# Optimization experiments

Hardware: AMD Instinct MI355X
Metric: run time of the kernel (lower is better)

Reference implementation:

```python
import jax, jax.numpy as jnp
import numpy as np

DIM = 1024
HEADS = 16
DIM_HEAD = 64
CHUNK = 64
INNER = HEADS * DIM_HEAD  # 1024


def setup_inputs() -> dict:
    key = jax.random.key(0)
    k1, k2, k3 = jax.random.split(key, 3)
    x = jax.random.normal(k1, (4, 4096, DIM), dtype=jnp.float32)
    # nn.Linear weights stored as (out, in); apply as x @ W.T
    w_qkv = jax.random.normal(k2, (INNER * 3, DIM), dtype=jnp.float32) * (DIM ** -0.5)
    w_out = jax.random.normal(k3, (DIM, INNER), dtype=jnp.float32) * (INNER ** -0.5)
    b_out = jnp.zeros((DIM,), dtype=jnp.float32)
    return {"x": x, "w_qkv": w_qkv, "w_out": w_out, "b_out": b_out}


def reference(x, w_qkv, w_out, b_out):
    b, n, _ = x.shape
    scale = DIM_HEAD ** -0.5
    qkv = jnp.einsum('bnd,ed->bne', x, w_qkv)  # (b, n, 3*inner)
    q, k, v = jnp.split(qkv, 3, axis=-1)
    nblk = n // CHUNK

    def to_blocks(t):
        # (b, n, h*d) -> (b, h, nblk, c, d)
        t = t.reshape(b, n, HEADS, DIM_HEAD).transpose(0, 2, 1, 3)
        return t.reshape(b, HEADS, nblk, CHUNK, DIM_HEAD)

    qb, kb, vb = to_blocks(q), to_blocks(k), to_blocks(v)
    scores = jnp.einsum('bhgqd,bhgkd->bhgqk', qb, kb) * scale  # block-local
    attn = jax.nn.softmax(scores, axis=-1)
    ob = jnp.einsum('bhgqk,bhgkd->bhgqd', attn, vb)
    out = ob.reshape(b, HEADS, n, DIM_HEAD).transpose(0, 2, 1, 3).reshape(b, n, INNER)
    return jnp.einsum('bne,de->bnd', out, w_out) + b_out
```

## Files before the change

kernel.cpp:

```cpp
#include <hip/hip_runtime.h>
#include <stdint.h>

typedef __attribute__((ext_vector_type(8))) short bf16x8;
typedef __attribute__((ext_vector_type(4))) float f32x4;

__device__ __forceinline__ unsigned short bf16_of(float f) {
  union { float f; uint32_t u; } x; x.f = f;
  uint32_t r = x.u + 0x7fffu + ((x.u >> 16) & 1u);
  return (unsigned short)(r >> 16);
}

#define GLD16(gp, lp) __builtin_amdgcn_global_load_lds( \
    (const __attribute__((address_space(1))) uint32_t*)(gp), \
    (__attribute__((address_space(3))) uint32_t*)(lp), 16, 0, 0)

#define BAR() do { asm volatile("" ::: "memory"); __builtin_amdgcn_s_barrier(); asm volatile("" ::: "memory"); } while (0)

__global__ void cvt_f32_bf16(const float* __restrict__ src,
                             unsigned short* __restrict__ dst, int n4) {
  int i = blockIdx.x * blockDim.x + threadIdx.x;
  int stride = gridDim.x * blockDim.x;
  for (int j = i; j < n4; j += stride) {
    float4 f = ((const float4*)src)[j];
    union { unsigned short s[4]; uint2 v; } u;
    u.s[0] = bf16_of(f.x); u.s[1] = bf16_of(f.y);
    u.s[2] = bf16_of(f.z); u.s[3] = bf16_of(f.w);
    ((uint2*)dst)[j] = u.v;
  }
}

template<int BIAS, int OUTF32, int GW, int NSEG>
__global__ __launch_bounds__(512, 2)
void gemm256f(const unsigned short* __restrict__ A,
              const unsigned short* __restrict__ B,
              void* __restrict__ C, const float* __restrict__ bias,
              int N, int K)
{
  __shared__ __align__(1024) unsigned short sm[65536];
  char* const smb = (char*)sm;
  const int tid = threadIdx.x, w = tid >> 6, lane = tid & 63;
  const int wm = w >> 2, wn = w & 3;
  const int fr = lane & 15, kg = lane >> 4;
  const int swz = (fr & 7) << 4;
  const int srow = lane >> 3, sslot = lane & 7;
  const int cXcd = blockIdx.x & 7, iIdx = blockIdx.x >> 3;
  const int NT_tot = NSEG * 16;

  auto tileMN = [&](int s, int& mt, int& nt) {
    const int T = cXcd * (32 * NSEG) + s * 32 + iIdx;
    const int g = T / (64 * GW), rr = T % (64 * GW);
    mt = rr / GW; nt = g * GW + rr % GW;
  };

  auto STAGE = [&](int u, int opnd, int half) {
    int mt, nt; tileMN(u >> 4, mt, nt);
    const unsigned short* G_ = opnd ? B : A;
    const int grow0 = (opnd ? nt : mt) << 8;
    char* region = smb + opnd * 65536 + (u & 1) * 32768 + half * 16384;
    const int k0 = (u & 15) << 6;
    #pragma unroll
    for (int i2 = 0; i2 < 2; ++i2) {
      const int c = i2 * 8 + w;
      const int row = half * 128 + c * 8 + srow;
      const int slot = sslot ^ srow;
      GLD16(G_ + (size_t)(grow0 + row) * K + k0 + slot * 8, region + c * 1024);
    }
  };
  auto LDA = [&](char* Ab, int j, int ks) -> bf16x8 {
    const int r = 32 * j + 16 * wm + fr;
    return *(const bf16x8*)(Ab + r * 128 + ((ks * 64 + kg * 16) ^ swz));
  };
  auto LDB = [&](char* Bb, int l, int ks) -> bf16x8 {
    const int r = 64 * l + 16 * wn + fr;
    return *(const bf16x8*)(Bb + r * 128 + ((ks * 64 + kg * 16) ^ swz));
  };

  f32x4 acc[8][4] = {};

  STAGE(0, 1, 0); STAGE(0, 0, 0); STAGE(0, 1, 1); STAGE(0, 0, 1);

  for (int s = 0; s < NSEG; ++s) {
    for (int tt = 0; tt < 16; ++tt) {
      const int T = s * 16 + tt;
      char* Ab = smb + (T & 1) * 32768;
      char* Bb = smb + 65536 + (T & 1) * 32768;
      bf16x8 a[4][2], b0[2][2], b1[2][2];

      asm volatile("s_waitcnt vmcnt(2)" ::: "memory");
      BAR();

      if (T + 1 < NT_tot) {
        STAGE(T + 1, 1, 0);
        STAGE(T + 1, 0, 0);
        STAGE(T + 1, 1, 1);
        STAGE(T + 1, 0, 1);
      }

      #pragma unroll
      for (int l = 0; l < 2; ++l) { b0[l][0] = LDB(Bb, l, 0); b0[l][1] = LDB(Bb, l, 1); }
      #pragma unroll
      for (int j = 0; j < 4; ++j) { a[j][0] = LDA(Ab, j, 0); a[j][1] = LDA(Ab, j, 1); }
      #pragma unroll
      for (int l = 0; l < 2; ++l) { b1[l][0] = LDB(Bb, l + 2, 0); b1[l][1] = LDB(Bb, l + 2, 1); }
      __builtin_amdgcn_s_setprio(1);
      #pragma unroll
      for (int j = 0; j < 4; ++j)
        #pragma unroll
        for (int l = 0; l < 2; ++l) {
          acc[j][l] = __builtin_amdgcn_mfma_f32_16x16x32_bf16(a[j][0], b0[l][0], acc[j][l], 0, 0, 0);
          acc[j][l] = __builtin_amdgcn_mfma_f32_16x16x32_bf16(a[j][1], b0[l][1], acc[j][l], 0, 0, 0);
        }
      #pragma unroll
      for (int j = 0; j < 4; ++j)
        #pragma unroll
        for (int l = 0; l < 2; ++l) {
          acc[j][l + 2] = __builtin_amdgcn_mfma_f32_16x16x32_bf16(a[j][0], b1[l][0], acc[j][l + 2], 0, 0, 0);
          acc[j][l + 2] = __builtin_amdgcn_mfma_f32_16x16x32_bf16(a[j][1], b1[l][1], acc[j][l + 2], 0, 0, 0);
        }
      __builtin_amdgcn_s_setprio(0);

      asm volatile("s_waitcnt vmcnt(8)" ::: "memory");
      BAR();

      #pragma unroll
      for (int j = 0; j < 4; ++j) { a[j][0] = LDA(Ab, j + 4, 0); a[j][1] = LDA(Ab, j + 4, 1); }
      __builtin_amdgcn_s_setprio(1);
      #pragma unroll
      for (int j = 0; j < 4; ++j)
        #pragma unroll
        for (int l = 0; l < 2; ++l) {
          acc[j + 4][l + 2] = __builtin_amdgcn_mfma_f32_16x16x32_bf16(a[j][0], b1[l][0], acc[j + 4][l + 2], 0, 0, 0);
          acc[j + 4][l + 2] = __builtin_amdgcn_mfma_f32_16x16x32_bf16(a[j][1], b1[l][1], acc[j + 4][l + 2], 0, 0, 0);
        }
      #pragma unroll
      for (int j = 0; j < 4; ++j)
        #pragma unroll
        for (int l = 0; l < 2; ++l) {
          acc[j + 4][l] = __builtin_amdgcn_mfma_f32_16x16x32_bf16(a[j][0], b0[l][0], acc[j + 4][l], 0, 0, 0);
          acc[j + 4][l] = __builtin_amdgcn_mfma_f32_16x16x32_bf16(a[j][1], b0[l][1], acc[j + 4][l], 0, 0, 0);
        }
      __builtin_amdgcn_s_setprio(0);
    }

    int mt, nt; tileMN(s, mt, nt);
    const int bm0 = mt << 8, bn0 = nt << 8;
    #pragma unroll
    for (int l = 0; l < 4; ++l) {
      const int col = bn0 + 64 * l + 16 * wn + fr;
      float bb = 0.0f;
      if (BIAS && OUTF32) bb = bias[col];
      #pragma unroll
      for (int j = 0; j < 8; ++j) {
        const int row0 = bm0 + 32 * j + 16 * wm + kg * 4;
        #pragma unroll
        for (int rr = 0; rr < 4; ++rr) {
          if (OUTF32)
            ((float*)C)[(size_t)(row0 + rr) * N + col] = acc[j][l][rr] + bb;
          else
            ((unsigned short*)C)[(size_t)(row0 + rr) * N + col] = bf16_of(acc[j][l][rr]);
        }
      }
    }
    #pragma unroll
    for (int j = 0; j < 8; ++j)
      #pragma unroll
      for (int l = 0; l < 4; ++l)
        acc[j][l] = f32x4{0.f, 0.f, 0.f, 0.f};
  }
}

__global__ __launch_bounds__(256, 2)
void attn_block(const unsigned short* __restrict__ qkv,
                unsigned short* __restrict__ o)
{
  __shared__ __align__(1024) unsigned short Qs[64 * 64];
  __shared__ __align__(1024) unsigned short Ks[64 * 64];
  __shared__ __align__(1024) unsigned short Vt[64 * 64];
  __shared__ __align__(1024) unsigned short Ps[64 * 64];
  const int tid = threadIdx.x, w = tid >> 6, lane = tid & 63;
  const int g = blockIdx.x, h = blockIdx.y, b = blockIdx.z;
  const size_t mbase = (size_t)b * 4096 + (size_t)g * 64;
  const unsigned short* qg = qkv + mbase * 3072 + h * 64;
  const unsigned short* kgl = qkv + mbase * 3072 + 1024 + h * 64;
  const unsigned short* vg = qkv + mbase * 3072 + 2048 + h * 64;

  #pragma unroll
  for (int i = 0; i < 2; ++i) {
    const int chunk = i * 4 + w;
    const int row = chunk * 8 + (lane >> 3);
    const int c8 = (lane & 7) ^ (row & 7);
    GLD16(qg + (size_t)row * 3072 + c8 * 8, (char*)Qs + chunk * 1024);
    GLD16(kgl + (size_t)row * 3072 + c8 * 8, (char*)Ks + chunk * 1024);
  }
  #pragma unroll
  for (int i = 0; i < 2; ++i) {
    const int c = i * 256 + tid;
    const int n = c >> 3, d0 = (c & 7) * 8;
    bf16x8 v = *(const bf16x8*)(vg + (size_t)n * 3072 + d0);
    #pragma unroll
    for (int j = 0; j < 8; ++j) {
      const int d = d0 + j;
      const int bo = d * 128 + n * 2;
      *(unsigned short*)((char*)Vt + (bo ^ ((d & 7) << 4))) = (unsigned short)v[j];
    }
  }
  __syncthreads();

  const int fr = lane & 15, kg = lane >> 4;
  f32x4 s[4] = {};
  #pragma unroll
  for (int kt = 0; kt < 2; ++kt) {
    const int kb = kt * 64 + kg * 16;
    const int rq = w * 16 + fr;
    bf16x8 aq = *(const bf16x8*)((const char*)Qs + rq * 128 + (kb ^ ((rq & 7) << 4)));
    #pragma unroll
    for (int nf = 0; nf < 4; ++nf) {
      const int rk = nf * 16 + fr;
      bf16x8 bk = *(const bf16x8*)((const char*)Ks + rk * 128 + (kb ^ ((rk & 7) << 4)));
      s[nf] = __builtin_amdgcn_mfma_f32_16x16x32_bf16(aq, bk, s[nf], 0, 0, 0);
    }
  }

  const float scale = 0.125f;
  float inv[4];
  #pragma unroll
  for (int r = 0; r < 4; ++r) {
    float m0 = fmaxf(fmaxf(s[0][r], s[1][r]), fmaxf(s[2][r], s[3][r]));
    #pragma unroll
    for (int d = 1; d < 16; d <<= 1) m0 = fmaxf(m0, __shfl_xor(m0, d));
    float sum = 0.0f;
    #pragma unroll
    for (int nf = 0; nf < 4; ++nf) {
      float p = __expf((s[nf][r] - m0) * scale);
      s[nf][r] = p;
      sum += p;
    }
    #pragma unroll
    for (int d = 1; d < 16; d <<= 1) sum += __shfl_xor(sum, d);
    inv[r] = 1.0f / sum;
  }

  #pragma unroll
  for (int r = 0; r < 4; ++r) {
    const int m = w * 16 + kg * 4 + r;
    #pragma unroll
    for (int nf = 0; nf < 4; ++nf) {
      const int bo = m * 128 + (nf * 16 + fr) * 2;
      *(unsigned short*)((char*)Ps + (bo ^ ((m & 7) << 4))) = bf16_of(s[nf][r] * inv[r]);
    }
  }
  __syncthreads();

  f32x4 oa[4] = {};
  #pragma unroll
  for (int kt = 0; kt < 2; ++kt) {
    const int kb = kt * 64 + kg * 16;
    const int rp = w * 16 + fr;
    bf16x8 ap = *(const bf16x8*)((const char*)Ps + rp * 128 + (kb ^ ((rp & 7) << 4)));
    #pragma unroll
    for (int df = 0; df < 4; ++df) {
      const int rv = df * 16 + fr;
      bf16x8 bv = *(const bf16x8*)((const char*)Vt + rv * 128 + (kb ^ ((rv & 7) << 4)));
      oa[df] = __builtin_amdgcn_mfma_f32_16x16x32_bf16(ap, bv, oa[df], 0, 0, 0);
    }
  }
  #pragma unroll
  for (int df = 0; df < 4; ++df) {
    #pragma unroll
    for (int r = 0; r < 4; ++r) {
      const size_t row = mbase + w * 16 + kg * 4 + r;
      const int col = h * 64 + df * 16 + fr;
      o[row * 1024 + col] = bf16_of(oa[df][r]);
    }
  }
}

extern "C" void kernel_launch(void* const* d_in, const int* in_sizes, int n_in,
                              void* d_out, int out_size, void* d_ws, size_t ws_size,
                              hipStream_t stream) {
  const float* x     = (const float*)d_in[0];
  const float* w_qkv = (const float*)d_in[1];
  const float* w_out = (const float*)d_in[2];
  const float* b_out = (const float*)d_in[3];
  char* ws = (char*)d_ws;
  const size_t SZ_X  = (size_t)16384 * 1024 * 2;
  const size_t SZ_WQ = (size_t)3072 * 1024 * 2;
  const size_t SZ_WO = (size_t)1024 * 1024 * 2;
  unsigned short* xb  = (unsigned short*)ws;
  unsigned short* wqb = (unsigned short*)(ws + SZ_X);
  unsigned short* wob = (unsigned short*)(ws + SZ_X + SZ_WQ);
  unsigned short* qkv = (unsigned short*)(ws + SZ_X + SZ_WQ + SZ_WO);
  unsigned short* ob  = xb;

  cvt_f32_bf16<<<2048, 256, 0, stream>>>(x, xb, 16384 * 1024 / 4);
  cvt_f32_bf16<<<512, 256, 0, stream>>>(w_qkv, wqb, 3072 * 1024 / 4);
  cvt_f32_bf16<<<256, 256, 0, stream>>>(w_out, wob, 1024 * 1024 / 4);
  gemm256f<0,0,6,3><<<dim3(256), 512, 0, stream>>>(xb, wqb, qkv, nullptr, 3072, 1024);
  attn_block<<<dim3(64, 16, 4), 256, 0, stream>>>(qkv, ob);
  gemm256f<1,1,4,1><<<dim3(256), 512, 0, stream>>>(ob, wob, d_out, b_out, 1024, 1024);
}
```

Before: 185.4 us.

## Switch GEMM to 32x32x16 MFMA tiles and precompute staging offsets

Rewrites the persistent GEMM inner loop to use 32x32x16 bf16 MFMA instructions with 32-row fragments instead of 16x16x32, changing the LDS fragment layout and the epilogue row mapping. This gives fewer, larger MFMAs and fewer LDS reads per FLOP. Staging addresses are now precomputed per thread and segment base pointers carried forward, which removes repeated tile index math in the load path. It also drains vmcnt fully on the last iteration. The risk is different register pressure and LDS bank behavior with the new swizzle.

```diff
diff --git a/kernel.cpp b/kernel.cpp
--- a/kernel.cpp
+++ b/kernel.cpp
@@ -3,6 +3,7 @@
 
 typedef __attribute__((ext_vector_type(8))) short bf16x8;
 typedef __attribute__((ext_vector_type(4))) float f32x4;
+typedef __attribute__((ext_vector_type(16))) float f32x16;
 
 __device__ __forceinline__ unsigned short bf16_of(float f) {
   union { float f; uint32_t u; } x; x.f = f;
@@ -31,7 +32,7 @@
 
 template<int BIAS, int OUTF32, int GW, int NSEG>
 __global__ __launch_bounds__(512, 2)
-void gemm256f(const unsigned short* __restrict__ A,
+void gemm256g(const unsigned short* __restrict__ A,
               const unsigned short* __restrict__ B,
               void* __restrict__ C, const float* __restrict__ bias,
               int N, int K)
@@ -40,8 +41,7 @@
   char* const smb = (char*)sm;
   const int tid = threadIdx.x, w = tid >> 6, lane = tid & 63;
   const int wm = w >> 2, wn = w & 3;
-  const int fr = lane & 15, kg = lane >> 4;
-  const int swz = (fr & 7) << 4;
+  const int lane31 = lane & 31, l5 = lane >> 5;
   const int srow = lane >> 3, sslot = lane & 7;
   const int cXcd = blockIdx.x & 7, iIdx = blockIdx.x >> 3;
   const int NT_tot = NSEG * 16;
@@ -52,120 +52,143 @@
     mt = rr / GW; nt = g * GW + rr % GW;
   };
 
-  auto STAGE = [&](int u, int opnd, int half) {
-    int mt, nt; tileMN(u >> 4, mt, nt);
-    const unsigned short* G_ = opnd ? B : A;
-    const int grow0 = (opnd ? nt : mt) << 8;
-    char* region = smb + opnd * 65536 + (u & 1) * 32768 + half * 16384;
-    const int k0 = (u & 15) << 6;
-    #pragma unroll
-    for (int i2 = 0; i2 < 2; ++i2) {
-      const int c = i2 * 8 + w;
-      const int row = half * 128 + c * 8 + srow;
-      const int slot = sslot ^ srow;
-      GLD16(G_ + (size_t)(grow0 + row) * K + k0 + slot * 8, region + c * 1024);
-    }
+  int stOff[2][2];
+  #pragma unroll
+  for (int h = 0; h < 2; ++h)
+    #pragma unroll
+    for (int i2 = 0; i2 < 2; ++i2)
+      stOff[h][i2] = (h * 128 + (i2 * 8 + w) * 8 + srow) * K + (sslot ^ srow) * 8;
+
+  int curMt, curNt, nxtMt, nxtNt;
+  tileMN(0, curMt, curNt);
+  nxtMt = curMt; nxtNt = curNt;
+  if (NSEG > 1) tileMN(1, nxtMt, nxtNt);
+  const unsigned short* aSeg  = A + ((size_t)curMt << 8) * K;
+  const unsigned short* bSeg  = B + ((size_t)curNt << 8) * K;
+  const unsigned short* aSegN = A + ((size_t)nxtMt << 8) * K;
+  const unsigned short* bSegN = B + ((size_t)nxtNt << 8) * K;
+
+  auto STAGEh = [&](const unsigned short* src, int opnd, int half, int parity) {
+    char* region = smb + opnd * 65536 + parity * 32768 + half * 16384;
+    GLD16(src + stOff[half][0], region + w * 1024);
+    GLD16(src + stOff[half][1], region + (8 + w) * 1024);
   };
-  auto LDA = [&](char* Ab, int j, int ks) -> bf16x8 {
-    const int r = 32 * j + 16 * wm + fr;
-    return *(const bf16x8*)(Ab + r * 128 + ((ks * 64 + kg * 16) ^ swz));
+  auto LDA32 = [&](char* Ab, int j, int ks) -> bf16x8 {
+    const int r = 64 * j + 32 * wm + lane31;
+    return *(const bf16x8*)(Ab + r * 128 + ((ks * 32 + l5 * 16) ^ ((r & 7) << 4)));
   };
-  auto LDB = [&](char* Bb, int l, int ks) -> bf16x8 {
-    const int r = 64 * l + 16 * wn + fr;
-    return *(const bf16x8*)(Bb + r * 128 + ((ks * 64 + kg * 16) ^ swz));
+  auto LDB32 = [&](char* Bb, int l, int ks) -> bf16x8 {
+    const int r = 128 * l + 32 * wn + lane31;
+    return *(const bf16x8*)(Bb + r * 128 + ((ks * 32 + l5 * 16) ^ ((r & 7) << 4)));
   };
 
-  f32x4 acc[8][4] = {};
-
-  STAGE(0, 1, 0); STAGE(0, 0, 0); STAGE(0, 1, 1); STAGE(0, 0, 1);
+  f32x16 acc[4][2] = {};
+
+  STAGEh(bSeg, 1, 0, 0);
+  STAGEh(aSeg, 0, 0, 0);
+  STAGEh(bSeg, 1, 1, 0);
+  STAGEh(aSeg, 0, 1, 0);
 
   for (int s = 0; s < NSEG; ++s) {
     for (int tt = 0; tt < 16; ++tt) {
       const int T = s * 16 + tt;
       char* Ab = smb + (T & 1) * 32768;
       char* Bb = smb + 65536 + (T & 1) * 32768;
-      bf16x8 a[4][2], b0[2][2], b1[2][2];
 
       asm volatile("s_waitcnt vmcnt(2)" ::: "memory");
       BAR();
 
       if (T + 1 < NT_tot) {
-        STAGE(T + 1, 1, 0);
-        STAGE(T + 1, 0, 0);
-        STAGE(T + 1, 1, 1);
-        STAGE(T + 1, 0, 1);
+        const int p1 = (T + 1) & 1;
+        const unsigned short *aS, *bS;
+        if (tt < 15) { aS = aSeg + ((tt + 1) << 6); bS = bSeg + ((tt + 1) << 6); }
+        else         { aS = aSegN;                  bS = bSegN; }
+        STAGEh(bS, 1, 0, p1);
+        STAGEh(aS, 0, 0, p1);
+        STAGEh(bS, 1, 1, p1);
+        STAGEh(aS, 0, 1, p1);
       }
 
-      #pragma unroll
-      for (int l = 0; l < 2; ++l) { b0[l][0] = LDB(Bb, l, 0); b0[l][1] = LDB(Bb, l, 1); }
-      #pragma unroll
-      for (int j = 0; j < 4; ++j) { a[j][0] = LDA(Ab, j, 0); a[j][1] = LDA(Ab, j, 1); }
-      #pragma unroll
-      for (int l = 0; l < 2; ++l) { b1[l][0] = LDB(Bb, l + 2, 0); b1[l][1] = LDB(Bb, l + 2, 1); }
+      bf16x8 a[2][4], bb0[4], bb1[4];
+      #pragma unroll
+      for (int ks = 0; ks < 4; ++ks) bb0[ks] = LDB32(Bb, 0, ks);
+      #pragma unroll
+      for (int j = 0; j < 2; ++j)
+        #pragma unroll
+        for (int ks = 0; ks < 4; ++ks) a[j][ks] = LDA32(Ab, j, ks);
+      #pragma unroll
+      for (int ks = 0; ks < 4; ++ks) bb1[ks] = LDB32(Bb, 1, ks);
+
       __builtin_amdgcn_s_setprio(1);
       #pragma unroll
-      for (int j = 0; j < 4; ++j)
-        #pragma unroll
-        for (int l = 0; l < 2; ++l) {
-          acc[j][l] = __builtin_amdgcn_mfma_f32_16x16x32_bf16(a[j][0], b0[l][0], acc[j][l], 0, 0, 0);
-          acc[j][l] = __builtin_amdgcn_mfma_f32_16x16x32_bf16(a[j][1], b0[l][1], acc[j][l], 0, 0, 0);
-        }
-      #pragma unroll
-      for (int j = 0; j < 4; ++j)
-        #pragma unroll
-        for (int l = 0; l < 2; ++l) {
-          acc[j][l + 2] = __builtin_amdgcn_mfma_f32_16x16x32_bf16(a[j][0], b1[l][0], acc[j][l + 2], 0, 0, 0);
-          acc[j][l + 2] = __builtin_amdgcn_mfma_f32_16x16x32_bf16(a[j][1], b1[l][1], acc[j][l + 2], 0, 0, 0);
-        }
+      for (int j = 0; j < 2; ++j)
+        #pragma unroll
+        for (int ks = 0; ks < 4; ++ks)
+          acc[j][0] = __builtin_amdgcn_mfma_f32_32x32x16_bf16(a[j][ks], bb0[ks], acc[j][0], 0, 0, 0);
+      #pragma unroll
+      for (int j = 0; j < 2; ++j)
+        #pragma unroll
+        for (int ks = 0; ks < 4; ++ks)
+          acc[j][1] = __builtin_amdgcn_mfma_f32_32x32x16_bf16(a[j][ks], bb1[ks], acc[j][1], 0, 0, 0);
       __builtin_amdgcn_s_setprio(0);
 
-      asm volatile("s_waitcnt vmcnt(8)" ::: "memory");
+      if (T + 1 < NT_tot) asm volatile("s_waitcnt vmcnt(8)" ::: "memory");
+      else                asm volatile("s_waitcnt vmcnt(0)" ::: "memory");
       BAR();
 
       #pragma unroll
-      for (int j = 0; j < 4; ++j) { a[j][0] = LDA(Ab, j + 4, 0); a[j][1] = LDA(Ab, j + 4, 1); }
+      for (int j = 0; j < 2; ++j)
+        #pragma unroll
+        for (int ks = 0; ks < 4; ++ks) a[j][ks] = LDA32(Ab, j + 2, ks);
+
       __builtin_amdgcn_s_setprio(1);
       #pragma unroll
-      for (int j = 0; j < 4; ++j)
-        #pragma unroll
-        for (int l = 0; l < 2; ++l) {
-          acc[j + 4][l + 2] = __builtin_amdgcn_mfma_f32_16x16x32_bf16(a[j][0], b1[l][0], acc[j + 4][l + 2], 0, 0, 0);
-          acc[j + 4][l + 2] = __builtin_amdgcn_mfma_f32_16x16x32_bf16(a[j][1], b1[l][1], acc[j + 4][l + 2], 0, 0, 0);
-        }
-      #pragma unroll
-      for (int j = 0; j < 4; ++j)
-        #pragma unroll
-        for (int l = 0; l < 2; ++l) {
-          acc[j + 4][l] = __builtin_amdgcn_mfma_f32_16x16x32_bf16(a[j][0], b0[l][0], acc[j + 4][l], 0, 0, 0);
-          acc[j + 4][l] = __builtin_amdgcn_mfma_f32_16x16x32_bf16(a[j][1], b0[l][1], acc[j + 4][l], 0, 0, 0);
-        }
+      for (int j = 0; j < 2; ++j)
+        #pragma unroll
+        for (int ks = 0; ks < 4; ++ks)
+          acc[j + 2][1] = __builtin_amdgcn_mfma_f32_32x32x16_bf16(a[j][ks], bb1[ks], acc[j + 2][1], 0, 0, 0);
+      #pragma unroll
+      for (int j = 0; j < 2; ++j)
+        #pragma unroll
+        for (int ks = 0; ks < 4; ++ks)
+          acc[j + 2][0] = __builtin_amdgcn_mfma_f32_32x32x16_bf16(a[j][ks], bb0[ks], acc[j + 2][0], 0, 0, 0);
       __builtin_amdgcn_s_setprio(0);
     }
 
-    int mt, nt; tileMN(s, mt, nt);
-    const int bm0 = mt << 8, bn0 = nt << 8;
-    #pragma unroll
-    for (int l = 0; l < 4; ++l) {
-      const int col = bn0 + 64 * l + 16 * wn + fr;
+    const int bm0 = curMt << 8, bn0 = curNt << 8;
+    #pragma unroll
+    for (int l = 0; l < 2; ++l) {
+      const int col = bn0 + 128 * l + 32 * wn + lane31;
       float bb = 0.0f;
       if (BIAS && OUTF32) bb = bias[col];
       #pragma unroll
-      for (int j = 0; j < 8; ++j) {
-        const int row0 = bm0 + 32 * j + 16 * wm + kg * 4;
-        #pragma unroll
-        for (int rr = 0; rr < 4; ++rr) {
+      for (int j = 0; j < 4; ++j) {
+        const int row0 = bm0 + 64 * j + 32 * wm + 4 * l5;
+        #pragma unroll
+        for (int reg = 0; reg < 16; ++reg) {
+          const int row = row0 + (reg & 3) + 8 * (reg >> 2);
           if (OUTF32)
-            ((float*)C)[(size_t)(row0 + rr) * N + col] = acc[j][l][rr] + bb;
+            ((float*)C)[(size_t)row * N + col] = acc[j][l][reg] + bb;
           else
-            ((unsigned short*)C)[(size_t)(row0 + rr) * N + col] = bf16_of(acc[j][l][rr]);
+            ((unsigned short*)C)[(size_t)row * N + col] = bf16_of(acc[j][l][reg]);
         }
       }
     }
     #pragma unroll
-    for (int j = 0; j < 8; ++j)
-      #pragma unroll
-      for (int l = 0; l < 4; ++l)
-        acc[j][l] = f32x4{0.f, 0.f, 0.f, 0.f};
+    for (int j = 0; j < 4; ++j)
+      #pragma unroll
+      for (int l = 0; l < 2; ++l)
+        #pragma unroll
+        for (int reg = 0; reg < 16; ++reg)
+          acc[j][l][reg] = 0.0f;
+
+    curMt = nxtMt; curNt = nxtNt;
+    aSeg = aSegN; bSeg = bSegN;
+    if (s + 2 < NSEG) {
+      tileMN(s + 2, nxtMt, nxtNt);
+      aSegN = A + ((size_t)nxtMt << 8) * K;
+      bSegN = B + ((size_t)nxtNt << 8) * K;
+    }
   }
 }
 
@@ -295,7 +318,7 @@
   cvt_f32_bf16<<<2048, 256, 0, stream>>>(x, xb, 16384 * 1024 / 4);
   cvt_f32_bf16<<<512, 256, 0, stream>>>(w_qkv, wqb, 3072 * 1024 / 4);
   cvt_f32_bf16<<<256, 256, 0, stream>>>(w_out, wob, 1024 * 1024 / 4);
-  gemm256f<0,0,6,3><<<dim3(256), 512, 0, stream>>>(xb, wqb, qkv, nullptr, 3072, 1024);
+  gemm256g<0,0,6,3><<<dim3(256), 512, 0, stream>>>(xb, wqb, qkv, nullptr, 3072, 1024);
   attn_block<<<dim3(64, 16, 4), 256, 0, stream>>>(qkv, ob);
-  gemm256f<1,1,4,1><<<dim3(256), 512, 0, stream>>>(ob, wob, d_out, b_out, 1024, 1024);
-}
+  gemm256g<1,1,4,1><<<dim3(256), 512, 0, stream>>>(ob, wob, d_out, b_out, 1024, 1024);
+}
```

Measured after the change: 205.7 us. 11.0% more time.
